# Optimization experiments

Measured on AMD Instinct MI355X. Metric: run time of the kernel, lower is better.

## Reference

```python
import jax, jax.numpy as jnp
import numpy as np

ROI = 7  # roi_size


def _conv1x1_softmax_fuse(a, b, w, bias):
    # a, b: (..., C, H, W); w: (2, 2C); bias: (2,)
    cat = jnp.concatenate([a, b], axis=-3)
    logits = jnp.einsum('oc,...chw->...ohw', w, cat) + bias[:, None, None]
    att = jax.nn.softmax(logits, axis=-3)
    return a * att[..., 0:1, :, :] + b * att[..., 1:2, :, :]


def _roi_align(feat, anchors):
    # torchvision RoIAlign (aligned=False, spatial_scale=1, sampling_ratio=-1).
    # Box width == ROI exactly -> bin size 1, adaptive grid = 1 sample per bin
    # at bin center: sample point = anchor - ROI/2 + (p + 0.5), p in [0, ROI).
    # feat: (C,H,W), anchors: (N,2) -> (N,C,ROI,ROI)
    C, H, W = feat.shape
    N = anchors.shape[0]
    half = ROI / 2.0
    offs = jnp.arange(ROI, dtype=feat.dtype) + 0.5
    sx = anchors[:, 0, None] - half + offs  # (N, ROI)
    sy = anchors[:, 1, None] - half + offs
    X = jnp.broadcast_to(sx[:, None, :], (N, ROI, ROI)).reshape(-1)  # pw fastest
    Y = jnp.broadcast_to(sy[:, :, None], (N, ROI, ROI)).reshape(-1)
    valid = (X >= -1.0) & (X <= W) & (Y >= -1.0) & (Y <= H)
    x = jnp.maximum(X, 0.0)
    y = jnp.maximum(Y, 0.0)
    x0 = jnp.floor(x).astype(jnp.int32)
    y0 = jnp.floor(y).astype(jnp.int32)
    xl = jnp.minimum(x0, W - 1)
    xh = jnp.minimum(x0 + 1, W - 1)
    yl = jnp.minimum(y0, H - 1)
    yh = jnp.minimum(y0 + 1, H - 1)
    lx = jnp.where(x0 >= W - 1, 0.0, x - xl)
    ly = jnp.where(y0 >= H - 1, 0.0, y - yl)
    hx, hy = 1.0 - lx, 1.0 - ly
    v = (feat[:, yl, xl] * (hy * hx) + feat[:, yl, xh] * (hy * lx)
         + feat[:, yh, xl] * (ly * hx) + feat[:, yh, xh] * (ly * lx))  # (C, P)
    v = jnp.where(valid, v, 0.0)
    return v.reshape(C, N, ROI, ROI).transpose(1, 0, 2, 3)


def _scatter_rois(base, rois, x0, y0):
    # sequential per-anchor overwrite of ROIxROI patches, matching torch loop order
    def step(m, args):
        roi, xx, yy = args
        return jax.lax.dynamic_update_slice(m, roi, (0, yy, xx)), None
    out, _ = jax.lax.scan(step, base, (rois, x0, y0))
    return out


def _forward(feat_rgb, feat_tir, a_rgb_c, a_tir_c, w_global, b_global, w_att, b_att):
    anchors_rgb = jax.lax.stop_gradient(a_rgb_c[..., :2])
    anchors_tir = jax.lax.stop_gradient(a_tir_c[..., :2])
    # GlobalFeatureFusion == per-pixel 1x1 conv + softmax-2 blend
    fused_global = _conv1x1_softmax_fuse(feat_rgb, feat_tir, w_global, b_global)
    rgb_rois = jax.vmap(_roi_align)(feat_rgb, anchors_rgb)  # (B,N,C,r,r)
    tir_rois = jax.vmap(_roi_align)(feat_tir, anchors_tir)
    fused_rois = _conv1x1_softmax_fuse(rgb_rois, tir_rois, w_att, b_att)
    fused_rois = jax.lax.stop_gradient(fused_rois)  # .detach() in fuse_rois_to_map
    H, W = feat_rgb.shape[2], feat_rgb.shape[3]
    half = ROI / 2.0
    x0 = jnp.clip(jnp.trunc(anchors_rgb[..., 0] - half).astype(jnp.int32), 0, W - ROI)
    y0 = jnp.clip(jnp.trunc(anchors_rgb[..., 1] - half).astype(jnp.int32), 0, H - ROI)
    return jax.vmap(_scatter_rois)(fused_global, fused_rois, x0, y0)


def setup_inputs():
    key = jax.random.key(0)
    ks = jax.random.split(key, 10)
    B, C, H, W, N = 8, 256, 128, 128, 128
    half = ROI / 2.0
    feat_rgb = jax.random.normal(ks[0], (B, C, H, W), dtype=jnp.float32)
    feat_tir = jax.random.normal(ks[1], (B, C, H, W), dtype=jnp.float32)

    def anchors(kx, ky, kc):
        ax = jax.random.uniform(kx, (B, N), minval=half, maxval=W - half)
        ay = jax.random.uniform(ky, (B, N), minval=half, maxval=H - half)
        cf = jax.random.uniform(kc, (B, N))
        return jnp.stack([ax, ay, cf], axis=-1).astype(jnp.float32)

    a_rgb = anchors(ks[2], ks[3], ks[4])
    a_tir = anchors(ks[5], ks[6], ks[7])
    w_global = jax.random.normal(ks[8], (2, 2 * C), dtype=jnp.float32) * 0.05
    b_global = jnp.zeros((2,), dtype=jnp.float32)
    w_att = jax.random.normal(ks[9], (2, 2 * C), dtype=jnp.float32) * 0.05
    b_att = jnp.zeros((2,), dtype=jnp.float32)
    return {"feat_rgb": feat_rgb, "feat_tir": feat_tir,
            "anchors_rgb_with_conf": a_rgb, "anchors_tir_with_conf": a_tir,
            "w_global": w_global, "b_global": b_global,
            "w_att": w_att, "b_att": b_att}


def reference(feat_rgb, feat_tir, anchors_rgb_with_conf, anchors_tir_with_conf,
              w_global, b_global, w_att, b_att):
    return _forward(feat_rgb, feat_tir, anchors_rgb_with_conf, anchors_tir_with_conf,
                    w_global, b_global, w_att, b_att)
```

## Files before the change

### kernel.cpp

```cpp
#include <hip/hip_runtime.h>
#include <math.h>

#define ROI 7
#define NC 256
#define TC 512
#define HH 128
#define WW 128
#define HW (HH * WW)

__global__ void init_owner_k(int* __restrict__ owner, int n) {
    int i = blockIdx.x * blockDim.x + threadIdx.x;
    if (i < n) owner[i] = -1;
}

__global__ void mark_owner_k(const float* __restrict__ anchors,
                             int* __restrict__ owner, int B, int N) {
    int i = blockIdx.x * blockDim.x + threadIdx.x;
    int total = B * N * 49;
    if (i >= total) return;
    int p = i % 49;
    int bn = i / 49;
    int n = bn % N;
    int b = bn / N;
    float ax = anchors[(size_t)(b * N + n) * 3 + 0];
    float ay = anchors[(size_t)(b * N + n) * 3 + 1];
    int x0 = (int)truncf(ax - 3.5f); x0 = min(max(x0, 0), WW - ROI);
    int y0 = (int)truncf(ay - 3.5f); y0 = min(max(y0, 0), HH - ROI);
    int x = x0 + (p % 7);
    int y = y0 + (p / 7);
    atomicMax(&owner[((size_t)b << 14) + (y << 7) + x], n);
}

struct BW { float w00, w01, w10, w11; };

__device__ inline BW bilin_weights(float X, float Y) {
    BW r;
    bool valid = (X >= -1.0f) && (X <= (float)WW) && (Y >= -1.0f) && (Y <= (float)HH);
    float x = fmaxf(X, 0.0f), y = fmaxf(Y, 0.0f);
    int ix = (int)floorf(x), iy = (int)floorf(y);
    int xl = min(ix, WW - 1);
    int yl = min(iy, HH - 1);
    float lx = (ix >= WW - 1) ? 0.0f : x - (float)xl;
    float ly = (iy >= HH - 1) ? 0.0f : y - (float)yl;
    float hx = 1.0f - lx, hy = 1.0f - ly;
    float s = valid ? 1.0f : 0.0f;
    r.w00 = hy * hx * s; r.w01 = hy * lx * s;
    r.w10 = ly * hx * s; r.w11 = ly * lx * s;
    return r;
}

__global__ __launch_bounds__(512) void fused_k(
        const float* __restrict__ rgb, const float* __restrict__ tir,
        const float* __restrict__ a_rgb, const float* __restrict__ a_tir,
        const float* __restrict__ wg, const float* __restrict__ bg,
        const float* __restrict__ wa, const float* __restrict__ ba,
        const int* __restrict__ owner, float* __restrict__ out,
        int N, int nRoi, int nFuse) {
    __shared__ float w[2 * TC];
    __shared__ float part0[64][9];
    __shared__ float part1[64][9];
    __shared__ float att[64];

    int bid = blockIdx.x;
    int tid = threadIdx.x;

    bool isRoi;
    int idx;
    if (nFuse == 2 * nRoi) {
        int q = bid / 3, r = bid - 3 * q;
        isRoi = (r == 0);
        idx = isRoi ? q : (bid - q - 1);
    } else {
        isRoi = (bid < nRoi);
        idx = isRoi ? bid : (bid - nRoi);
    }

    int p  = tid & 63;
    int g  = tid >> 6;
    int c0 = g << 5;

    if (isRoi) {
        int b = idx / N, n = idx % N;
        for (int i = tid; i < 2 * TC; i += 512) w[i] = wa[i];

        int lx = p & 7, ly = p >> 3;
        bool isPt = (lx < 7) && (ly < 7);

        float axr = a_rgb[(size_t)(b * N + n) * 3 + 0];
        float ayr = a_rgb[(size_t)(b * N + n) * 3 + 1];
        float axt = a_tir[(size_t)(b * N + n) * 3 + 0];
        float ayt = a_tir[(size_t)(b * N + n) * 3 + 1];

        int gx0r = max(0, (int)floorf(axr - 3.0f));
        int gy0r = max(0, (int)floorf(ayr - 3.0f));
        int gx0t = max(0, (int)floorf(axt - 3.0f));
        int gy0t = max(0, (int)floorf(ayt - 3.0f));
        int offr = (min(gy0r + ly, HH - 1) << 7) + min(gx0r + lx, WW - 1);
        int offt = (min(gy0t + ly, HH - 1) << 7) + min(gx0t + lx, WW - 1);

        float Xr = (axr - 3.5f) + ((float)lx + 0.5f);
        float Yr = (ayr - 3.5f) + ((float)ly + 0.5f);
        float Xt = (axt - 3.5f) + ((float)lx + 0.5f);
        float Yt = (ayt - 3.5f) + ((float)ly + 0.5f);
        BW br = bilin_weights(Xr, Yr);
        BW bt = bilin_weights(Xt, Yt);

        int x0 = (int)truncf(axr - 3.5f); x0 = min(max(x0, 0), WW - ROI);
        int y0 = (int)truncf(ayr - 3.5f); y0 = min(max(y0, 0), HH - ROI);
        int x = x0 + lx, y = y0 + ly;
        bool act = isPt;
        if (act) act = (owner[((size_t)b << 14) + (y << 7) + x] == n);

        const float* rb = rgb + (((size_t)b * NC) << 14);
        const float* tb = tir + (((size_t)b * NC) << 14);

        __syncthreads();

        float vr[32], vt[32];
        float l0 = 0.f, l1 = 0.f;
        #pragma unroll
        for (int i = 0; i < 32; ++i) {
            int c = c0 + i;
            float gr0 = rb[((size_t)c << 14) + offr];
            float gt0 = tb[((size_t)c << 14) + offt];
            float gr1 = __shfl_down(gr0, 1, 64);
            float gr8 = __shfl_down(gr0, 8, 64);
            float gr9 = __shfl_down(gr0, 9, 64);
            float gt1 = __shfl_down(gt0, 1, 64);
            float gt8 = __shfl_down(gt0, 8, 64);
            float gt9 = __shfl_down(gt0, 9, 64);
            vr[i] = br.w00 * gr0 + br.w01 * gr1 + br.w10 * gr8 + br.w11 * gr9;
            vt[i] = bt.w00 * gt0 + bt.w01 * gt1 + bt.w10 * gt8 + bt.w11 * gt9;
            l0 = fmaf(w[c],          vr[i], fmaf(w[NC + c],     vt[i], l0));
            l1 = fmaf(w[2 * NC + c], vr[i], fmaf(w[3 * NC + c], vt[i], l1));
        }
        part0[p][g] = l0;
        part1[p][g] = l1;
        __syncthreads();
        if (g == 0 && isPt) {
            float L0 = ba[0], L1 = ba[1];
            #pragma unroll
            for (int s = 0; s < 8; ++s) { L0 += part0[p][s]; L1 += part1[p][s]; }
            float m = fmaxf(L0, L1);
            float e0 = expf(L0 - m), e1 = expf(L1 - m);
            att[p] = e0 / (e0 + e1);
        }
        __syncthreads();
        if (!act) return;

        float a0 = att[p];
        float* po = out + (((size_t)b * NC) << 14) + (y << 7) + x;
        #pragma unroll
        for (int i = 0; i < 32; ++i) {
            int c = c0 + i;
            po[(size_t)c << 14] = fmaf(a0, vr[i] - vt[i], vt[i]);
        }
    } else {
        int b = idx >> 8;
        int pix = ((idx & 255) << 6) + p;
        for (int i = tid; i < 2 * TC; i += 512) w[i] = wg[i];

        bool act = owner[((size_t)b << 14) + pix] < 0;

        const float* pr = rgb + (((size_t)b * NC) << 14) + pix;
        const float* pt = tir + (((size_t)b * NC) << 14) + pix;

        __syncthreads();

        float vr[32], vt[32];
        if (act) {
            float l0 = 0.f, l1 = 0.f;
            #pragma unroll
            for (int i = 0; i < 32; ++i) {
                int c = c0 + i;
                vr[i] = pr[(size_t)c << 14];
                vt[i] = pt[(size_t)c << 14];
                l0 = fmaf(w[c],          vr[i], fmaf(w[NC + c],     vt[i], l0));
                l1 = fmaf(w[2 * NC + c], vr[i], fmaf(w[3 * NC + c], vt[i], l1));
            }
            part0[p][g] = l0;
            part1[p][g] = l1;
        }
        __syncthreads();
        if (g == 0 && act) {
            float L0 = bg[0], L1 = bg[1];
            #pragma unroll
            for (int s = 0; s < 8; ++s) { L0 += part0[p][s]; L1 += part1[p][s]; }
            float m = fmaxf(L0, L1);
            float e0 = expf(L0 - m), e1 = expf(L1 - m);
            att[p] = e0 / (e0 + e1);
        }
        __syncthreads();
        if (!act) return;

        float a0 = att[p];
        float* po = out + (((size_t)b * NC) << 14) + pix;
        #pragma unroll
        for (int i = 0; i < 32; ++i) {
            int c = c0 + i;
            po[(size_t)c << 14] = fmaf(a0, vr[i] - vt[i], vt[i]);
        }
    }
}

extern "C" void kernel_launch(void* const* d_in, const int* in_sizes, int n_in,
                              void* d_out, int out_size, void* d_ws, size_t ws_size,
                              hipStream_t stream) {
    const float* frgb = (const float*)d_in[0];
    const float* ftir = (const float*)d_in[1];
    const float* argb = (const float*)d_in[2];
    const float* atir = (const float*)d_in[3];
    const float* wg   = (const float*)d_in[4];
    const float* bgp  = (const float*)d_in[5];
    const float* wa   = (const float*)d_in[6];
    const float* bap  = (const float*)d_in[7];
    float* out = (float*)d_out;

    int B = in_sizes[0] / (NC * HW);
    int N = in_sizes[2] / (B * 3);
    int npix = B * HW;
    int nRoi = B * N;
    int nFuse = npix / 64;

    int* owner = (int*)d_ws;

    init_owner_k<<<(npix + 255) / 256, 256, 0, stream>>>(owner, npix);
    mark_owner_k<<<(B * N * 49 + 255) / 256, 256, 0, stream>>>(argb, owner, B, N);
    fused_k<<<nRoi + nFuse, 512, 0, stream>>>(frgb, ftir, argb, atir,
                                              wg, bgp, wa, bap,
                                              owner, out, N, nRoi, nFuse);
}
```

Baseline: 188.2 us.

## Precompute per-pixel attention logits and interpolate them in separate ROI pass

The global fusion pass now writes every pixel unconditionally and also computes per-pixel partial logits for the ROI attention weights (rgb and tir projections), storing them as a float4 field in workspace. Because the 1x1 conv is linear, the ROI kernel bilinearly interpolates these precomputed logits instead of reducing over 512 channels, then does only the gather-interpolate-blend per channel and overwrites owned pixels. The single mixed launch is split into two kernels in sequence. This removes the cross-warp logit reduction and shared-memory syncs from ROI blocks and the owner check in the fuse blocks, at the cost of extra workspace traffic, redundant writes of pixels later overwritten by ROIs, and a serialising kernel boundary.

```diff
diff --git a/kernel.cpp b/kernel.cpp
--- a/kernel.cpp
+++ b/kernel.cpp
@@ -31,175 +31,154 @@
     atomicMax(&owner[((size_t)b << 14) + (y << 7) + x], n);
 }
 
-struct BW { float w00, w01, w10, w11; };
-
-__device__ inline BW bilin_weights(float X, float Y) {
-    BW r;
-    bool valid = (X >= -1.0f) && (X <= (float)WW) && (Y >= -1.0f) && (Y <= (float)HH);
-    float x = fmaxf(X, 0.0f), y = fmaxf(Y, 0.0f);
-    int ix = (int)floorf(x), iy = (int)floorf(y);
-    int xl = min(ix, WW - 1);
-    int yl = min(iy, HH - 1);
-    float lx = (ix >= WW - 1) ? 0.0f : x - (float)xl;
-    float ly = (iy >= HH - 1) ? 0.0f : y - (float)yl;
-    float hx = 1.0f - lx, hy = 1.0f - ly;
-    float s = valid ? 1.0f : 0.0f;
-    r.w00 = hy * hx * s; r.w01 = hy * lx * s;
-    r.w10 = ly * hx * s; r.w11 = ly * lx * s;
-    return r;
-}
-
-__global__ __launch_bounds__(512) void fused_k(
+__device__ inline void axis_w(float X, int limit, float& w0, float& w1) {
+    float x = fmaxf(X, 0.0f);
+    int ix = (int)floorf(x);
+    float l = (ix >= limit - 1) ? 0.0f : x - (float)min(ix, limit - 1);
+    w0 = 1.0f - l;
+    w1 = l;
+}
+
+__global__ __launch_bounds__(512) void fuse_fields_k(
+        const float* __restrict__ rgb, const float* __restrict__ tir,
+        const float* __restrict__ wg, const float* __restrict__ bg,
+        const float* __restrict__ wa,
+        float* __restrict__ out, float4* __restrict__ lf) {
+    __shared__ float swg[2 * TC];
+    __shared__ float swa[2 * TC];
+    __shared__ float part[6][64][9];
+    __shared__ float att[64];
+
+    int tid = threadIdx.x;
+    int b = blockIdx.x >> 8;
+    int pix0 = (blockIdx.x & 255) << 6;
+    int px = tid & 63, g = tid >> 6, c0 = g << 5;
+
+    for (int i = tid; i < 2 * TC; i += 512) { swg[i] = wg[i]; swa[i] = wa[i]; }
+
+    const float* pr = rgb + (((size_t)b * NC) << 14) + pix0 + px;
+    const float* pt = tir + (((size_t)b * NC) << 14) + pix0 + px;
+
+    __syncthreads();
+
+    float vr[32], vt[32];
+    float lg0 = 0.f, lg1 = 0.f, f0r = 0.f, f1r = 0.f, f0t = 0.f, f1t = 0.f;
+    #pragma unroll
+    for (int i = 0; i < 32; ++i) {
+        int c = c0 + i;
+        vr[i] = pr[(size_t)c << 14];
+        vt[i] = pt[(size_t)c << 14];
+        lg0 = fmaf(swg[c],          vr[i], fmaf(swg[NC + c],     vt[i], lg0));
+        lg1 = fmaf(swg[2 * NC + c], vr[i], fmaf(swg[3 * NC + c], vt[i], lg1));
+        f0r = fmaf(swa[c],          vr[i], f0r);
+        f1r = fmaf(swa[2 * NC + c], vr[i], f1r);
+        f0t = fmaf(swa[NC + c],     vt[i], f0t);
+        f1t = fmaf(swa[3 * NC + c], vt[i], f1t);
+    }
+    part[0][px][g] = lg0; part[1][px][g] = lg1;
+    part[2][px][g] = f0r; part[3][px][g] = f1r;
+    part[4][px][g] = f0t; part[5][px][g] = f1t;
+    __syncthreads();
+
+    if (tid < 64) {
+        float s[6];
+        #pragma unroll
+        for (int k = 0; k < 6; ++k) {
+            float acc = 0.f;
+            #pragma unroll
+            for (int q = 0; q < 8; ++q) acc += part[k][tid][q];
+            s[k] = acc;
+        }
+        float L0 = bg[0] + s[0], L1 = bg[1] + s[1];
+        float m = fmaxf(L0, L1);
+        float e0 = expf(L0 - m), e1 = expf(L1 - m);
+        att[tid] = e0 / (e0 + e1);
+        lf[(size_t)b * HW + pix0 + tid] = make_float4(s[2], s[3], s[4], s[5]);
+    }
+    __syncthreads();
+
+    float a0 = att[px];
+    float* po = out + (((size_t)b * NC) << 14) + pix0 + px;
+    #pragma unroll
+    for (int i = 0; i < 32; ++i) {
+        int c = c0 + i;
+        po[(size_t)c << 14] = fmaf(a0, vr[i] - vt[i], vt[i]);
+    }
+}
+
+__global__ __launch_bounds__(512) void roi_k(
         const float* __restrict__ rgb, const float* __restrict__ tir,
         const float* __restrict__ a_rgb, const float* __restrict__ a_tir,
-        const float* __restrict__ wg, const float* __restrict__ bg,
-        const float* __restrict__ wa, const float* __restrict__ ba,
-        const int* __restrict__ owner, float* __restrict__ out,
-        int N, int nRoi, int nFuse) {
-    __shared__ float w[2 * TC];
-    __shared__ float part0[64][9];
-    __shared__ float part1[64][9];
-    __shared__ float att[64];
-
-    int bid = blockIdx.x;
+        const float* __restrict__ ba, const int* __restrict__ owner,
+        const float4* __restrict__ lf, float* __restrict__ out, int N) {
     int tid = threadIdx.x;
-
-    bool isRoi;
-    int idx;
-    if (nFuse == 2 * nRoi) {
-        int q = bid / 3, r = bid - 3 * q;
-        isRoi = (r == 0);
-        idx = isRoi ? q : (bid - q - 1);
-    } else {
-        isRoi = (bid < nRoi);
-        idx = isRoi ? bid : (bid - nRoi);
-    }
-
-    int p  = tid & 63;
-    int g  = tid >> 6;
-    int c0 = g << 5;
-
-    if (isRoi) {
-        int b = idx / N, n = idx % N;
-        for (int i = tid; i < 2 * TC; i += 512) w[i] = wa[i];
-
-        int lx = p & 7, ly = p >> 3;
-        bool isPt = (lx < 7) && (ly < 7);
-
-        float axr = a_rgb[(size_t)(b * N + n) * 3 + 0];
-        float ayr = a_rgb[(size_t)(b * N + n) * 3 + 1];
-        float axt = a_tir[(size_t)(b * N + n) * 3 + 0];
-        float ayt = a_tir[(size_t)(b * N + n) * 3 + 1];
-
-        int gx0r = max(0, (int)floorf(axr - 3.0f));
-        int gy0r = max(0, (int)floorf(ayr - 3.0f));
-        int gx0t = max(0, (int)floorf(axt - 3.0f));
-        int gy0t = max(0, (int)floorf(ayt - 3.0f));
-        int offr = (min(gy0r + ly, HH - 1) << 7) + min(gx0r + lx, WW - 1);
-        int offt = (min(gy0t + ly, HH - 1) << 7) + min(gx0t + lx, WW - 1);
-
-        float Xr = (axr - 3.5f) + ((float)lx + 0.5f);
-        float Yr = (ayr - 3.5f) + ((float)ly + 0.5f);
-        float Xt = (axt - 3.5f) + ((float)lx + 0.5f);
-        float Yt = (ayt - 3.5f) + ((float)ly + 0.5f);
-        BW br = bilin_weights(Xr, Yr);
-        BW bt = bilin_weights(Xt, Yt);
-
-        int x0 = (int)truncf(axr - 3.5f); x0 = min(max(x0, 0), WW - ROI);
-        int y0 = (int)truncf(ayr - 3.5f); y0 = min(max(y0, 0), HH - ROI);
-        int x = x0 + lx, y = y0 + ly;
-        bool act = isPt;
-        if (act) act = (owner[((size_t)b << 14) + (y << 7) + x] == n);
-
-        const float* rb = rgb + (((size_t)b * NC) << 14);
-        const float* tb = tir + (((size_t)b * NC) << 14);
-
-        __syncthreads();
-
-        float vr[32], vt[32];
-        float l0 = 0.f, l1 = 0.f;
-        #pragma unroll
-        for (int i = 0; i < 32; ++i) {
-            int c = c0 + i;
-            float gr0 = rb[((size_t)c << 14) + offr];
-            float gt0 = tb[((size_t)c << 14) + offt];
-            float gr1 = __shfl_down(gr0, 1, 64);
-            float gr8 = __shfl_down(gr0, 8, 64);
-            float gr9 = __shfl_down(gr0, 9, 64);
-            float gt1 = __shfl_down(gt0, 1, 64);
-            float gt8 = __shfl_down(gt0, 8, 64);
-            float gt9 = __shfl_down(gt0, 9, 64);
-            vr[i] = br.w00 * gr0 + br.w01 * gr1 + br.w10 * gr8 + br.w11 * gr9;
-            vt[i] = bt.w00 * gt0 + bt.w01 * gt1 + bt.w10 * gt8 + bt.w11 * gt9;
-            l0 = fmaf(w[c],          vr[i], fmaf(w[NC + c],     vt[i], l0));
-            l1 = fmaf(w[2 * NC + c], vr[i], fmaf(w[3 * NC + c], vt[i], l1));
-        }
-        part0[p][g] = l0;
-        part1[p][g] = l1;
-        __syncthreads();
-        if (g == 0 && isPt) {
-            float L0 = ba[0], L1 = ba[1];
-            #pragma unroll
-            for (int s = 0; s < 8; ++s) { L0 += part0[p][s]; L1 += part1[p][s]; }
-            float m = fmaxf(L0, L1);
-            float e0 = expf(L0 - m), e1 = expf(L1 - m);
-            att[p] = e0 / (e0 + e1);
-        }
-        __syncthreads();
-        if (!act) return;
-
-        float a0 = att[p];
-        float* po = out + (((size_t)b * NC) << 14) + (y << 7) + x;
-        #pragma unroll
-        for (int i = 0; i < 32; ++i) {
-            int c = c0 + i;
-            po[(size_t)c << 14] = fmaf(a0, vr[i] - vt[i], vt[i]);
-        }
-    } else {
-        int b = idx >> 8;
-        int pix = ((idx & 255) << 6) + p;
-        for (int i = tid; i < 2 * TC; i += 512) w[i] = wg[i];
-
-        bool act = owner[((size_t)b << 14) + pix] < 0;
-
-        const float* pr = rgb + (((size_t)b * NC) << 14) + pix;
-        const float* pt = tir + (((size_t)b * NC) << 14) + pix;
-
-        __syncthreads();
-
-        float vr[32], vt[32];
-        if (act) {
-            float l0 = 0.f, l1 = 0.f;
-            #pragma unroll
-            for (int i = 0; i < 32; ++i) {
-                int c = c0 + i;
-                vr[i] = pr[(size_t)c << 14];
-                vt[i] = pt[(size_t)c << 14];
-                l0 = fmaf(w[c],          vr[i], fmaf(w[NC + c],     vt[i], l0));
-                l1 = fmaf(w[2 * NC + c], vr[i], fmaf(w[3 * NC + c], vt[i], l1));
-            }
-            part0[p][g] = l0;
-            part1[p][g] = l1;
-        }
-        __syncthreads();
-        if (g == 0 && act) {
-            float L0 = bg[0], L1 = bg[1];
-            #pragma unroll
-            for (int s = 0; s < 8; ++s) { L0 += part0[p][s]; L1 += part1[p][s]; }
-            float m = fmaxf(L0, L1);
-            float e0 = expf(L0 - m), e1 = expf(L1 - m);
-            att[p] = e0 / (e0 + e1);
-        }
-        __syncthreads();
-        if (!act) return;
-
-        float a0 = att[p];
-        float* po = out + (((size_t)b * NC) << 14) + pix;
-        #pragma unroll
-        for (int i = 0; i < 32; ++i) {
-            int c = c0 + i;
-            po[(size_t)c << 14] = fmaf(a0, vr[i] - vt[i], vt[i]);
-        }
+    int b = blockIdx.x / N, n = blockIdx.x % N;
+    int p = tid & 63, wid = tid >> 6, c0 = wid << 5;
+    int lx = p & 7, ly = p >> 3;
+
+    float axr = a_rgb[(size_t)(b * N + n) * 3 + 0];
+    float ayr = a_rgb[(size_t)(b * N + n) * 3 + 1];
+    float axt = a_tir[(size_t)(b * N + n) * 3 + 0];
+    float ayt = a_tir[(size_t)(b * N + n) * 3 + 1];
+
+    int gx0r = max(0, (int)floorf(axr - 3.0f));
+    int gy0r = max(0, (int)floorf(ayr - 3.0f));
+    int gx0t = max(0, (int)floorf(axt - 3.0f));
+    int gy0t = max(0, (int)floorf(ayt - 3.0f));
+    int offr = (min(gy0r + ly, HH - 1) << 7) + min(gx0r + lx, WW - 1);
+    int offt = (min(gy0t + ly, HH - 1) << 7) + min(gx0t + lx, WW - 1);
+
+    float Xr = (axr - 3.5f) + ((float)lx + 0.5f);
+    float Yr = (ayr - 3.5f) + ((float)ly + 0.5f);
+    float Xt = (axt - 3.5f) + ((float)lx + 0.5f);
+    float Yt = (ayt - 3.5f) + ((float)ly + 0.5f);
+
+    float wxr0, wxr1, wyr0, wyr1, wxt0, wxt1, wyt0, wyt1;
+    axis_w(Xr, WW, wxr0, wxr1);
+    axis_w(Yr, HH, wyr0, wyr1);
+    axis_w(Xt, WW, wxt0, wxt1);
+    axis_w(Yt, HH, wyt0, wyt1);
+    bool vldr = (Xr >= -1.0f) && (Xr <= (float)WW) && (Yr >= -1.0f) && (Yr <= (float)HH);
+    bool vldt = (Xt >= -1.0f) && (Xt <= (float)WW) && (Yt >= -1.0f) && (Yt <= (float)HH);
+    float sr = vldr ? 1.0f : 0.0f;
+    float st = vldt ? 1.0f : 0.0f;
+
+    int x0 = (int)truncf(axr - 3.5f); x0 = min(max(x0, 0), WW - ROI);
+    int y0 = (int)truncf(ayr - 3.5f); y0 = min(max(y0, 0), HH - ROI);
+    int x = x0 + lx, y = y0 + ly;
+    bool act = (lx < 7) && (ly < 7);
+    if (act) act = (owner[((size_t)b << 14) + (y << 7) + x] == n);
+
+    float4 Fr = lf[(size_t)b * HW + offr];
+    float4 Ft = lf[(size_t)b * HW + offt];
+    float h0 = wxr0 * Fr.x + wxr1 * __shfl_down(Fr.x, 1, 64);
+    float G0r = wyr0 * h0 + wyr1 * __shfl_down(h0, 8, 64);
+    float h1 = wxr0 * Fr.y + wxr1 * __shfl_down(Fr.y, 1, 64);
+    float G1r = wyr0 * h1 + wyr1 * __shfl_down(h1, 8, 64);
+    float h2 = wxt0 * Ft.z + wxt1 * __shfl_down(Ft.z, 1, 64);
+    float G0t = wyt0 * h2 + wyt1 * __shfl_down(h2, 8, 64);
+    float h3 = wxt0 * Ft.w + wxt1 * __shfl_down(Ft.w, 1, 64);
+    float G1t = wyt0 * h3 + wyt1 * __shfl_down(h3, 8, 64);
+    float L0 = ba[0] + sr * G0r + st * G0t;
+    float L1 = ba[1] + sr * G1r + st * G1t;
+    float m = fmaxf(L0, L1);
+    float e0 = expf(L0 - m), e1 = expf(L1 - m);
+    float a0 = e0 / (e0 + e1);
+
+    const float* rb = rgb + (((size_t)b * NC) << 14);
+    const float* tb = tir + (((size_t)b * NC) << 14);
+    float* po = out + (((size_t)b * NC) << 14) + (y << 7) + x;
+    #pragma unroll
+    for (int i = 0; i < 32; ++i) {
+        int c = c0 + i;
+        float gr = rb[((size_t)c << 14) + offr];
+        float gt = tb[((size_t)c << 14) + offt];
+        float hr = wxr0 * gr + wxr1 * __shfl_down(gr, 1, 64);
+        float vvr = wyr0 * hr + wyr1 * __shfl_down(hr, 8, 64);
+        float ht = wxt0 * gt + wxt1 * __shfl_down(gt, 1, 64);
+        float vvt = wyt0 * ht + wyt1 * __shfl_down(ht, 8, 64);
+        float vr = sr * vvr, vt = st * vvt;
+        if (act) po[(size_t)c << 14] = fmaf(a0, vr - vt, vt);
     }
 }
 
@@ -219,14 +198,13 @@
     int B = in_sizes[0] / (NC * HW);
     int N = in_sizes[2] / (B * 3);
     int npix = B * HW;
-    int nRoi = B * N;
-    int nFuse = npix / 64;
 
     int* owner = (int*)d_ws;
+    float4* lf = (float4*)((char*)d_ws + (size_t)npix * 4);
 
     init_owner_k<<<(npix + 255) / 256, 256, 0, stream>>>(owner, npix);
     mark_owner_k<<<(B * N * 49 + 255) / 256, 256, 0, stream>>>(argb, owner, B, N);
-    fused_k<<<nRoi + nFuse, 512, 0, stream>>>(frgb, ftir, argb, atir,
-                                              wg, bgp, wa, bap,
-                                              owner, out, N, nRoi, nFuse);
-}
+    fuse_fields_k<<<npix / 64, 512, 0, stream>>>(frgb, ftir, wg, bgp, wa, out, lf);
+    roi_k<<<B * N, 512, 0, stream>>>(frgb, ftir, argb, atir, bap,
+                                     owner, lf, out, N);
+}
```

After: 207.1 us. 1.1x slower.
